# Performance work log

Hardware: AMD Instinct MI355X
Metric: run time of the kernel (lower is better)

The kernel has to match this reference:

```python
import math
import jax, jax.numpy as jnp
import numpy as np

V, BS, L, C, H, B, T = 50257, 2048, 4, 768, 12, 2, 2048
D = C // H


def layer_norm(x, g, b, eps=1e-5):
    m = x.mean(-1, keepdims=True)
    v = ((x - m) ** 2).mean(-1, keepdims=True)
    return (x - m) / jnp.sqrt(v + eps) * g + b


def setup_inputs() -> dict:
    key = jax.random.key(0)
    ks = jax.random.split(key, 10)
    s = 0.02
    inp = {}
    inp["idx"] = jax.random.randint(ks[0], (B, T), 0, V)
    inp["tok_emb"] = jax.random.normal(ks[1], (V, C), jnp.float32) * s
    inp["pos_emb"] = jax.random.normal(ks[2], (BS, C), jnp.float32) * s
    inp["ln1_g"] = jnp.ones((L, C)); inp["ln1_b"] = jnp.zeros((L, C))
    inp["qkv_w"] = jax.random.normal(ks[3], (L, C, 3 * C), jnp.float32) * s
    inp["qkv_b"] = jnp.zeros((L, 3 * C))
    inp["aproj_w"] = jax.random.normal(ks[4], (L, C, C), jnp.float32) * s
    inp["aproj_b"] = jnp.zeros((L, C))
    inp["ln2_g"] = jnp.ones((L, C)); inp["ln2_b"] = jnp.zeros((L, C))
    inp["fc_w"] = jax.random.normal(ks[5], (L, C, 4 * C), jnp.float32) * s
    inp["fc_b"] = jnp.zeros((L, 4 * C))
    inp["mproj_w"] = jax.random.normal(ks[6], (L, 4 * C, C), jnp.float32) * s
    inp["mproj_b"] = jnp.zeros((L, C))
    inp["lnf_g"] = jnp.ones((C,)); inp["lnf_b"] = jnp.zeros((C,))
    inp["head_w"] = jax.random.normal(ks[7], (C, V), jnp.float32) * s
    return inp


def reference(idx, tok_emb, pos_emb, ln1_g, ln1_b, qkv_w, qkv_b, aproj_w, aproj_b,
              ln2_g, ln2_b, fc_w, fc_b, mproj_w, mproj_b, lnf_g, lnf_b, head_w):
    b, t = idx.shape
    x = tok_emb[idx] + pos_emb[:t][None]  # [B,T,C]; dropout p=0 -> identity
    mask = jnp.tril(jnp.ones((t, t), bool))  # causal
    neg_inf = jnp.finfo(x.dtype).min
    n_layer = qkv_w.shape[0]
    for l in range(n_layer):
        h = layer_norm(x, ln1_g[l], ln1_b[l])
        qkv = h @ qkv_w[l] + qkv_b[l]  # [B,T,3C]
        q, k, v = jnp.split(qkv, 3, axis=-1)
        q = q.reshape(b, t, H, D).transpose(0, 2, 1, 3)  # [B,H,T,D]
        k = k.reshape(b, t, H, D).transpose(0, 2, 1, 3)
        v = v.reshape(b, t, H, D).transpose(0, 2, 1, 3)
        att = jnp.einsum('bhqd,bhkd->bhqk', q, k) / math.sqrt(D)
        att = jnp.where(mask, att, neg_inf)
        att = jax.nn.softmax(att, axis=-1)
        y = jnp.einsum('bhqk,bhkd->bhqd', att, v)
        y = y.transpose(0, 2, 1, 3).reshape(b, t, C)
        x = x + (y @ aproj_w[l] + aproj_b[l])
        h2 = layer_norm(x, ln2_g[l], ln2_b[l])
        hid = jax.nn.gelu(h2 @ fc_w[l] + fc_b[l], approximate=False)  # exact erf GELU (torch default)
        x = x + (hid @ mproj_w[l] + mproj_b[l])
    x = layer_norm(x, lnf_g, lnf_b)
    logits = x @ head_w  # [B,T,V]
    return logits
```

## Files before the change

kernel.cpp:

```cpp
#include <hip/hip_runtime.h>
#include <cstdint>
#include <cstddef>

#define Tn 2048
#define Bn 2
#define Hn 12
#define Cn 768
#define Ln 4
#define Vn 50257

typedef unsigned short ushort_t;
typedef __attribute__((ext_vector_type(8))) __bf16 bf16x8;
typedef __attribute__((ext_vector_type(8))) unsigned short u16x8;
typedef __attribute__((ext_vector_type(4))) float f32x4;

static constexpr size_t QKV_ELEMS = (size_t)Bn * Hn * Tn * 64;

__device__ inline unsigned short f2bf(float f) {
  unsigned int u = __float_as_uint(f);
  unsigned int r = (u + 0x7fffu + ((u >> 16) & 1u)) >> 16;
  return (unsigned short)r;
}

__device__ inline f32x4 zero4() { f32x4 z; z[0]=0.f; z[1]=0.f; z[2]=0.f; z[3]=0.f; return z; }

__device__ inline void gload_lds16(const ushort_t* g, ushort_t* l) {
  __builtin_amdgcn_global_load_lds(
      (const __attribute__((address_space(1))) void*)g,
      (__attribute__((address_space(3))) void*)l, 16, 0, 0);
}

__device__ inline int swz_lin() {
  int nbm = gridDim.x;
  int lin = blockIdx.y * nbm + blockIdx.x;
  int nwg = nbm * gridDim.y;
  int q = nwg >> 3, r = nwg & 7, x = lin & 7, p = lin >> 3;
  return (x < r ? x * (q + 1) : r * (q + 1) + (x - r) * q) + p;
}

__global__ __launch_bounds__(256) void embed_kernel(const int* __restrict__ idx,
    const float* __restrict__ tok, const float* __restrict__ pos, float* __restrict__ x) {
  int row = blockIdx.x;
  int t = row & (Tn - 1);
  int token = idx[row];
  const float* tr = tok + (size_t)token * Cn;
  const float* pr = pos + (size_t)t * Cn;
  float* xr = x + (size_t)row * Cn;
  for (int c = threadIdx.x; c < Cn; c += 256) xr[c] = tr[c] + pr[c];
}

__global__ __launch_bounds__(256) void ln_kernel(const float* __restrict__ x,
    const float* __restrict__ gam, const float* __restrict__ bet, ushort_t* __restrict__ out) {
  int row = blockIdx.x;
  const float* xr = x + (size_t)row * Cn;
  float v[3]; float s = 0.f, s2 = 0.f;
  #pragma unroll
  for (int e = 0; e < 3; ++e) { float t = xr[threadIdx.x + e*256]; v[e] = t; s += t; s2 += t*t; }
  #pragma unroll
  for (int off = 32; off >= 1; off >>= 1) { s += __shfl_xor(s, off); s2 += __shfl_xor(s2, off); }
  __shared__ float red[8];
  int w = threadIdx.x >> 6;
  if ((threadIdx.x & 63) == 0) { red[w] = s; red[4 + w] = s2; }
  __syncthreads();
  s  = red[0] + red[1] + red[2] + red[3];
  s2 = red[4] + red[5] + red[6] + red[7];
  float mean = s * (1.f / Cn);
  float var  = s2 * (1.f / Cn) - mean * mean;
  float rstd = rsqrtf(var + 1e-5f);
  ushort_t* orow = out + (size_t)row * Cn;
  #pragma unroll
  for (int e = 0; e < 3; ++e) {
    int c = threadIdx.x + e*256;
    orow[c] = f2bf((v[e] - mean) * rstd * gam[c] + bet[c]);
  }
}

__global__ __launch_bounds__(256) void tcvt_kernel(const float* __restrict__ in,
    ushort_t* __restrict__ out, int K, int N, int Npad) {
  __shared__ float tile[32][33];
  int n0 = blockIdx.x * 32, k0 = blockIdx.y * 32;
  int tx = threadIdx.x, ty = threadIdx.y;
  #pragma unroll
  for (int r = 0; r < 4; ++r) {
    int k = k0 + ty + 8*r;
    int n = n0 + tx;
    tile[ty + 8*r][tx] = (n < N) ? in[(size_t)k * N + n] : 0.f;
  }
  __syncthreads();
  #pragma unroll
  for (int r = 0; r < 4; ++r) {
    int n = n0 + ty + 8*r;
    out[(size_t)n * K + k0 + tx] = f2bf(tile[tx][ty + 8*r]);
  }
}

__global__ __launch_bounds__(256) void vtrans_kernel(const ushort_t* __restrict__ vin,
                                                     ushort_t* __restrict__ vout) {
  __shared__ ushort_t tile[64][65];
  int t0 = blockIdx.x * 64;
  size_t bh = blockIdx.y;
  const ushort_t* src = vin + (bh * Tn + t0) * 64;
  int row = threadIdx.x >> 2, c0 = (threadIdx.x & 3) * 16;
  u16x8 a = *(const u16x8*)&src[(size_t)row * 64 + c0];
  u16x8 b = *(const u16x8*)&src[(size_t)row * 64 + c0 + 8];
  #pragma unroll
  for (int j = 0; j < 8; ++j) { tile[row][c0 + j] = a[j]; tile[row][c0 + 8 + j] = b[j]; }
  __syncthreads();
  int d = threadIdx.x >> 2, tq = (threadIdx.x & 3) * 16;
  u16x8 o0, o1;
  #pragma unroll
  for (int j = 0; j < 8; ++j) { o0[j] = tile[tq + j][d]; o1[j] = tile[tq + 8 + j][d]; }
  ushort_t* dst = vout + (bh * 64 + d) * Tn + t0 + tq;
  *(u16x8*)&dst[0] = o0;
  *(u16x8*)&dst[8] = o1;
}

__global__ __launch_bounds__(512, 2) void gemm256_kernel(
    const ushort_t* __restrict__ A, const ushort_t* __restrict__ Bt,
    const float* __restrict__ bias, float* __restrict__ outp,
    int M, int N, int K) {
  __shared__ ushort_t lds[3 * 16384];
  const int t = threadIdx.x;
  const int w = t >> 6, l = t & 63, lo = l & 15, g = l >> 4;
  const int wm = w >> 2, wn = w & 3;

  int bm, bn;
  {
    int seq = swz_lin();
    int gsz = 8 * gridDim.y;
    int grp = seq / gsz;
    int t2 = seq - grp * gsz;
    bn = t2 >> 3;
    bm = grp * 8 + (t2 & 7);
  }

  const ushort_t* gAb = A  + (size_t)bm * 256 * K;
  const ushort_t* gBb = Bt + (size_t)bn * 256 * K;

  f32x4 acc[8][4];
  #pragma unroll
  for (int i = 0; i < 8; ++i)
    #pragma unroll
    for (int j = 0; j < 4; ++j) acc[i][j] = zero4();

  auto stage = [&](int kt, int buf) {
    const int k0 = kt << 5;
    #pragma unroll
    for (int j = 0; j < 2; ++j) {
      const int q = j * 512 + t;
      const int r = q >> 2;
      const int cc = ((q & 3) ^ ((r >> 1) & 3)) << 3;
      gload_lds16(gAb + (size_t)r * K + k0 + cc,
                  &lds[buf * 16384 + j * 4096 + w * 512]);
      gload_lds16(gBb + (size_t)r * K + k0 + cc,
                  &lds[buf * 16384 + 8192 + j * 4096 + w * 512]);
    }
  };
  const int csw = ((lo >> 1) & 3) << 3;
  auto compute = [&](int buf) {
    const ushort_t* as = &lds[buf * 16384];
    const ushort_t* bs = &lds[buf * 16384 + 8192];
    bf16x8 af[8], bfr[4];
    #pragma unroll
    for (int mi = 0; mi < 8; ++mi)
      af[mi] = *(const bf16x8*)&as[(wm*128 + mi*16 + lo) * 32 + ((g*8) ^ csw)];
    #pragma unroll
    for (int ni = 0; ni < 4; ++ni)
      bfr[ni] = *(const bf16x8*)&bs[(wn*64 + ni*16 + lo) * 32 + ((g*8) ^ csw)];
    __builtin_amdgcn_s_setprio(1);
    #pragma unroll
    for (int mi = 0; mi < 8; ++mi)
      #pragma unroll
      for (int ni = 0; ni < 4; ++ni)
        acc[mi][ni] = __builtin_amdgcn_mfma_f32_16x16x32_bf16(af[mi], bfr[ni], acc[mi][ni], 0, 0, 0);
    __builtin_amdgcn_s_setprio(0);
  };

  const int NK = K >> 5;
  stage(0, 0); stage(1, 1); stage(2, 2);
  asm volatile("s_waitcnt vmcnt(8)" ::: "memory");
  __builtin_amdgcn_s_barrier();

  int buf = 0;
  #pragma unroll 1
  for (int kt = 0; kt < NK; ++kt) {
    compute(buf);
    asm volatile("s_waitcnt lgkmcnt(0)" ::: "memory");
    __builtin_amdgcn_s_barrier();
    if (kt + 3 < NK) {
      stage(kt + 3, buf);
      asm volatile("s_waitcnt vmcnt(8)" ::: "memory");
    } else if (kt + 2 < NK) {
      asm volatile("s_waitcnt vmcnt(4)" ::: "memory");
    } else {
      asm volatile("s_waitcnt vmcnt(0)" ::: "memory");
    }
    __builtin_amdgcn_s_barrier();
    buf = (buf == 2) ? 0 : buf + 1;
  }

  #pragma unroll
  for (int mi = 0; mi < 8; ++mi) {
    #pragma unroll
    for (int ni = 0; ni < 4; ++ni) {
      int colg = bn*256 + wn*64 + ni*16 + lo;
      if (colg < N) {
        float bv = bias ? bias[colg] : 0.f;
        #pragma unroll
        for (int i = 0; i < 4; ++i) {
          int rowg = bm*256 + wm*128 + mi*16 + 4*g + i;
          outp[(size_t)rowg * N + colg] = acc[mi][ni][i] + bv;
        }
      }
    }
  }
}

template<int MODE, int TM>
__global__ __launch_bounds__(256) void gemm_kernel(
    const ushort_t* __restrict__ A, const ushort_t* __restrict__ Bt,
    const float* __restrict__ bias, void* __restrict__ outp,
    const float* __restrict__ res, int M, int N, int K) {
  constexpr int MI = TM / 32;
  constexpr int ABUF = TM * 32;
  __shared__ ushort_t As[2 * ABUF];
  __shared__ ushort_t Bs[2 * 4096];
  const int t = threadIdx.x;
  int bm, bn;
  {
    int seq = swz_lin();
    const int G = 8;
    int NBN = gridDim.y;
    int gsz = G * NBN;
    int grp = seq / gsz;
    int t2 = seq - grp * gsz;
    bn = t2 / G;
    bm = grp * G + (t2 - bn * G);
  }
  const int w = t >> 6, l = t & 63, lo = l & 15, g = l >> 4;
  const int wm = w >> 1, wn = w & 1;

  f32x4 acc[MI][4];
  #pragma unroll
  for (int i = 0; i < MI; ++i)
    #pragma unroll
    for (int j = 0; j < 4; ++j) acc[i][j] = zero4();

  const int srow = t >> 2;
  const int scol = (t & 3) * 8;
  const ushort_t* gA = A  + (size_t)(bm * TM  + srow) * K + scol;
  const ushort_t* gB = Bt + (size_t)(bn * 128 + srow) * K + scol;
  ushort_t* lA = As + w * 512;
  ushort_t* lB = Bs + w * 512;

  auto stage = [&](int buf, int k0) {
    gload_lds16(gA + k0, lA + buf * ABUF);
    if (TM == 128) gload_lds16(gA + (size_t)64 * K + k0, lA + buf * ABUF + 2048);
    gload_lds16(gB + k0, lB + buf * 4096);
    gload_lds16(gB + (size_t)64 * K + k0, lB + buf * 4096 + 2048);
  };
  auto compute = [&](int buf) {
    const ushort_t* as = As + buf * ABUF;
    const ushort_t* bs = Bs + buf * 4096;
    bf16x8 af[MI], bfr[4];
    #pragma unroll
    for (int mi = 0; mi < MI; ++mi)
      af[mi] = *(const bf16x8*)&as[(size_t)(wm*(TM/2) + mi*16 + lo) * 32 + g*8];
    #pragma unroll
    for (int ni = 0; ni < 4; ++ni)
      bfr[ni] = *(const bf16x8*)&bs[(size_t)(wn*64 + ni*16 + lo) * 32 + g*8];
    #pragma unroll
    for (int mi = 0; mi < MI; ++mi)
      #pragma unroll
      for (int ni = 0; ni < 4; ++ni)
        acc[mi][ni] = __builtin_amdgcn_mfma_f32_16x16x32_bf16(af[mi], bfr[ni], acc[mi][ni], 0, 0, 0);
  };

  const int NK = K >> 5;
  stage(0, 0);
  __syncthreads();
  for (int kk = 0; kk < NK - 1; ++kk) {
    stage((kk + 1) & 1, (kk + 1) << 5);
    compute(kk & 1);
    __syncthreads();
  }
  compute((NK - 1) & 1);

  #pragma unroll
  for (int mi = 0; mi < MI; ++mi) {
    #pragma unroll
    for (int ni = 0; ni < 4; ++ni) {
      int colg = bn*128 + wn*64 + ni*16 + lo;
      if (colg < N) {
        float bv = bias ? bias[colg] : 0.f;
        #pragma unroll
        for (int i = 0; i < 4; ++i) {
          int rowg = bm*TM + wm*(TM/2) + mi*16 + 4*g + i;
          float vv = acc[mi][ni][i] + bv;
          if (MODE == 0) {
            ((float*)outp)[(size_t)rowg * N + colg] = vv;
          } else if (MODE == 1) {
            size_t off = (size_t)rowg * N + colg;
            ((float*)outp)[off] = res[off] + vv;
          } else if (MODE == 2) {
            float ge = 0.5f * vv * (1.f + erff(vv * 0.70710678118f));
            ((ushort_t*)outp)[(size_t)rowg * N + colg] = f2bf(ge);
          } else {
            int which = colg / Cn;
            int rem = colg - which * Cn;
            int h = rem >> 6, d = rem & 63;
            int b = rowg >> 11, tt = rowg & (Tn - 1);
            ushort_t* qb = (ushort_t*)outp;
            size_t bh = (size_t)(b * Hn + h);
            size_t off = (bh * Tn + tt) * 64 + d;
            if (which == 0)      qb[off] = f2bf(vv * 0.125f);
            else if (which == 1) qb[QKV_ELEMS + off] = f2bf(vv);
            else                 qb[3*QKV_ELEMS + off] = f2bf(vv);
          }
        }
      }
    }
  }
}

__global__ __launch_bounds__(64) void attn_kernel(const ushort_t* __restrict__ qkvh,
                                                  ushort_t* __restrict__ y) {
  const int l = threadIdx.x;
  const int lo = l & 15, g = l >> 4;
  int nl = swz_lin();
  const int qt = nl & 127;
  const int bh = nl >> 7;
  const int b = bh / Hn, h = bh % Hn;
  const int q0 = qt * 16;
  const ushort_t* Qp = qkvh + (size_t)bh * Tn * 64;
  const ushort_t* Kp = qkvh + QKV_ELEMS + (size_t)bh * Tn * 64;
  const ushort_t* Vt = qkvh + 2*QKV_ELEMS + (size_t)bh * 64 * Tn;

  bf16x8 qf[2];
  #pragma unroll
  for (int ch = 0; ch < 2; ++ch)
    qf[ch] = *(const bf16x8*)&Qp[(size_t)(q0 + lo) * 64 + ch*32 + g*8];

  f32x4 of[4];
  #pragma unroll
  for (int ch = 0; ch < 4; ++ch) of[ch] = zero4();
  float m = -1e30f, lsum = 0.f;
  const int nkv = q0 + 16;
  const bool ghi = (g >= 2);
  const int lg2 = (g & 1) * 32;

  for (int kv0 = 0; kv0 < nkv; kv0 += 32) {
    bf16x8 vf[4];
    #pragma unroll
    for (int ch = 0; ch < 4; ++ch)
      vf[ch] = *(const bf16x8*)&Vt[(size_t)(ch*16 + lo) * Tn + kv0 + g*8];

    float s8[8];
    #pragma unroll
    for (int sub = 0; sub < 2; ++sub) {
      int kvb = kv0 + 16*sub;
      bf16x8 kf[2];
      #pragma unroll
      for (int ch = 0; ch < 2; ++ch)
        kf[ch] = *(const bf16x8*)&Kp[(size_t)(kvb + lo) * 64 + ch*32 + g*8];
      f32x4 st = zero4();
      st = __builtin_amdgcn_mfma_f32_16x16x32_bf16(kf[0], qf[0], st, 0, 0, 0);
      st = __builtin_amdgcn_mfma_f32_16x16x32_bf16(kf[1], qf[1], st, 0, 0, 0);
      #pragma unroll
      for (int i = 0; i < 4; ++i) {
        int kvi = kvb + 4*g + i;
        s8[sub*4 + i] = (kvi <= q0 + lo) ? st[i] : -1e30f;
      }
    }
    float tmax = s8[0];
    #pragma unroll
    for (int j = 1; j < 8; ++j) tmax = fmaxf(tmax, s8[j]);
    tmax = fmaxf(tmax, __shfl_xor(tmax, 16));
    tmax = fmaxf(tmax, __shfl_xor(tmax, 32));
    if (!__all(tmax <= m)) {
      float newm = fmaxf(m, tmax);
      float resc = __expf(m - newm);
      lsum *= resc;
      m = newm;
      #pragma unroll
      for (int i = 0; i < 4; ++i) {
        float rs = __shfl(resc, 4*g + i);
        of[0][i] *= rs; of[1][i] *= rs; of[2][i] *= rs; of[3][i] *= rs;
      }
    }
    float p8[8]; float psum = 0.f;
    #pragma unroll
    for (int j = 0; j < 8; ++j) { p8[j] = __expf(s8[j] - m); psum += p8[j]; }
    psum += __shfl_xor(psum, 16);
    psum += __shfl_xor(psum, 32);
    lsum += psum;
    unsigned int q4[4];
    #pragma unroll
    for (int c = 0; c < 4; ++c)
      asm("v_cvt_pk_bf16_f32 %0, %1, %2" : "=v"(q4[c]) : "v"(p8[2*c]), "v"(p8[2*c+1]));
    union { unsigned int wv[4]; bf16x8 v; } pu;
    #pragma unroll
    for (int j = 0; j < 4; ++j) {
      int srcLane = lo + lg2 + ((j >> 1) << 4);
      unsigned int lo_w = (unsigned int)__shfl((int)q4[j & 1], srcLane);
      unsigned int hi_w = (unsigned int)__shfl((int)q4[2 + (j & 1)], srcLane);
      pu.wv[j] = ghi ? hi_w : lo_w;
    }
    #pragma unroll
    for (int ch = 0; ch < 4; ++ch)
      of[ch] = __builtin_amdgcn_mfma_f32_16x16x32_bf16(pu.v, vf[ch], of[ch], 0, 0, 0);
  }

  #pragma unroll
  for (int i = 0; i < 4; ++i) {
    float li = 1.f / __shfl(lsum, 4*g + i);
    of[0][i] *= li; of[1][i] *= li; of[2][i] *= li; of[3][i] *= li;
  }
  ushort_t* yb = y + ((size_t)b*Tn + q0) * Cn + h*64;
  #pragma unroll
  for (int ch = 0; ch < 4; ++ch)
    #pragma unroll
    for (int i = 0; i < 4; ++i)
      yb[(size_t)(4*g + i) * Cn + ch*16 + lo] = f2bf(of[ch][i]);
}

extern "C" void kernel_launch(void* const* d_in, const int* in_sizes, int n_in,
                              void* d_out, int out_size, void* d_ws, size_t ws_size,
                              hipStream_t stream) {
  const int*   idx     = (const int*)d_in[0];
  const float* tok_emb = (const float*)d_in[1];
  const float* pos_emb = (const float*)d_in[2];
  const float* ln1_g   = (const float*)d_in[3];
  const float* ln1_b   = (const float*)d_in[4];
  const float* qkv_w   = (const float*)d_in[5];
  const float* qkv_b   = (const float*)d_in[6];
  const float* aproj_w = (const float*)d_in[7];
  const float* aproj_b = (const float*)d_in[8];
  const float* ln2_g   = (const float*)d_in[9];
  const float* ln2_b   = (const float*)d_in[10];
  const float* fc_w    = (const float*)d_in[11];
  const float* fc_b    = (const float*)d_in[12];
  const float* mproj_w = (const float*)d_in[13];
  const float* mproj_b = (const float*)d_in[14];
  const float* lnf_g   = (const float*)d_in[15];
  const float* lnf_b   = (const float*)d_in[16];
  const float* head_w  = (const float*)d_in[17];
  float* out = (float*)d_out;

  char* ws = (char*)d_ws;
  float*    x    = (float*)(ws);
  ushort_t* hA   = (ushort_t*)(ws + 12582912);
  ushort_t* hB   = (ushort_t*)(ws + 18874368);
  ushort_t* qkvh = (ushort_t*)(ws + 44040192);
  ushort_t* wT   = (ushort_t*)(ws + 69206016);

  const int M = Bn * Tn;
  dim3 tb(32, 8);

  embed_kernel<<<M, 256, 0, stream>>>(idx, tok_emb, pos_emb, x);
  for (int l = 0; l < Ln; ++l) {
    ln_kernel<<<M, 256, 0, stream>>>(x, ln1_g + l*Cn, ln1_b + l*Cn, hA);
    tcvt_kernel<<<dim3(2304/32, 768/32), tb, 0, stream>>>(qkv_w + (size_t)l*Cn*3*Cn, wT, 768, 2304, 2304);
    gemm_kernel<3,128><<<dim3(M/128, 2304/128), 256, 0, stream>>>(hA, wT, qkv_b + (size_t)l*3*Cn, qkvh, nullptr, M, 2304, 768);
    vtrans_kernel<<<dim3(Tn/64, Bn*Hn), 256, 0, stream>>>(qkvh + 3*QKV_ELEMS, qkvh + 2*QKV_ELEMS);
    attn_kernel<<<dim3(128, Bn*Hn), 64, 0, stream>>>(qkvh, hA);
    tcvt_kernel<<<dim3(768/32, 768/32), tb, 0, stream>>>(aproj_w + (size_t)l*Cn*Cn, wT, 768, 768, 768);
    gemm_kernel<1,64><<<dim3(M/64, 768/128), 256, 0, stream>>>(hA, wT, aproj_b + (size_t)l*Cn, x, x, M, 768, 768);
    ln_kernel<<<M, 256, 0, stream>>>(x, ln2_g + l*Cn, ln2_b + l*Cn, hA);
    tcvt_kernel<<<dim3(3072/32, 768/32), tb, 0, stream>>>(fc_w + (size_t)l*Cn*4*Cn, wT, 768, 3072, 3072);
    gemm_kernel<2,128><<<dim3(M/128, 3072/128), 256, 0, stream>>>(hA, wT, fc_b + (size_t)l*4*Cn, hB, nullptr, M, 3072, 768);
    tcvt_kernel<<<dim3(768/32, 3072/32), tb, 0, stream>>>(mproj_w + (size_t)l*4*Cn*Cn, wT, 3072, 768, 768);
    gemm_kernel<1,64><<<dim3(M/64, 768/128), 256, 0, stream>>>(hB, wT, mproj_b + (size_t)l*Cn, x, x, M, 768, 3072);
  }
  ln_kernel<<<M, 256, 0, stream>>>(x, lnf_g, lnf_b, hA);
  tcvt_kernel<<<dim3(50432/32, 768/32), tb, 0, stream>>>(head_w, wT, 768, Vn, 50432);
  gemm256_kernel<<<dim3(M/256, 50432/256), 512, 0, stream>>>(hA, wT, nullptr, out, M, Vn, 768);
}
```

Before: 1.796 ms.

## Triple-buffer swizzled GEMM pipeline, batch weight conversion, vectorize LN and embed

The layer GEMM moves from a double-buffered LDS loop to a three-stage pipeline. It uses XOR-swizzled LDS layout, explicit vmcnt waits, raw barriers and s_setprio around the MFMA block, aiming to hide load latency and cut LDS bank conflicts. The four per-layer weight transpose/convert launches are merged into one launch writing to fixed offsets. LayerNorm now handles one row per wave with float4 loads and no shared-memory reduction, and the embedding kernel uses float4 loads. The hand-written waitcnt counts depend on how many loads each stage issues, so a wrong count would silently read stale LDS data.

```diff
diff --git a/kernel.cpp b/kernel.cpp
--- a/kernel.cpp
+++ b/kernel.cpp
@@ -12,9 +12,14 @@
 typedef unsigned short ushort_t;
 typedef __attribute__((ext_vector_type(8))) __bf16 bf16x8;
 typedef __attribute__((ext_vector_type(8))) unsigned short u16x8;
+typedef __attribute__((ext_vector_type(4))) unsigned short u16x4;
 typedef __attribute__((ext_vector_type(4))) float f32x4;
 
 static constexpr size_t QKV_ELEMS = (size_t)Bn * Hn * Tn * 64;
+static constexpr size_t OFF_QKV = 0;
+static constexpr size_t OFF_APROJ = 1769472;
+static constexpr size_t OFF_FC = 2359296;
+static constexpr size_t OFF_MPROJ = 4718592;
 
 __device__ inline unsigned short f2bf(float f) {
   unsigned int u = __float_as_uint(f);
@@ -38,40 +43,44 @@
   return (x < r ? x * (q + 1) : r * (q + 1) + (x - r) * q) + p;
 }
 
-__global__ __launch_bounds__(256) void embed_kernel(const int* __restrict__ idx,
+__global__ __launch_bounds__(192) void embed_kernel(const int* __restrict__ idx,
     const float* __restrict__ tok, const float* __restrict__ pos, float* __restrict__ x) {
   int row = blockIdx.x;
   int t = row & (Tn - 1);
   int token = idx[row];
-  const float* tr = tok + (size_t)token * Cn;
-  const float* pr = pos + (size_t)t * Cn;
-  float* xr = x + (size_t)row * Cn;
-  for (int c = threadIdx.x; c < Cn; c += 256) xr[c] = tr[c] + pr[c];
+  const f32x4* tr = (const f32x4*)(tok + (size_t)token * Cn);
+  const f32x4* pr = (const f32x4*)(pos + (size_t)t * Cn);
+  f32x4* xr = (f32x4*)(x + (size_t)row * Cn);
+  xr[threadIdx.x] = tr[threadIdx.x] + pr[threadIdx.x];
 }
 
 __global__ __launch_bounds__(256) void ln_kernel(const float* __restrict__ x,
     const float* __restrict__ gam, const float* __restrict__ bet, ushort_t* __restrict__ out) {
-  int row = blockIdx.x;
-  const float* xr = x + (size_t)row * Cn;
-  float v[3]; float s = 0.f, s2 = 0.f;
-  #pragma unroll
-  for (int e = 0; e < 3; ++e) { float t = xr[threadIdx.x + e*256]; v[e] = t; s += t; s2 += t*t; }
+  const int wv = threadIdx.x >> 6, lane = threadIdx.x & 63;
+  const int row = blockIdx.x * 4 + wv;
+  const f32x4* xr = (const f32x4*)(x + (size_t)row * Cn);
+  f32x4 v[3]; float s = 0.f, s2 = 0.f;
+  #pragma unroll
+  for (int e = 0; e < 3; ++e) {
+    v[e] = xr[lane + e*64];
+    #pragma unroll
+    for (int j = 0; j < 4; ++j) { s += v[e][j]; s2 += v[e][j]*v[e][j]; }
+  }
   #pragma unroll
   for (int off = 32; off >= 1; off >>= 1) { s += __shfl_xor(s, off); s2 += __shfl_xor(s2, off); }
-  __shared__ float red[8];
-  int w = threadIdx.x >> 6;
-  if ((threadIdx.x & 63) == 0) { red[w] = s; red[4 + w] = s2; }
-  __syncthreads();
-  s  = red[0] + red[1] + red[2] + red[3];
-  s2 = red[4] + red[5] + red[6] + red[7];
   float mean = s * (1.f / Cn);
   float var  = s2 * (1.f / Cn) - mean * mean;
   float rstd = rsqrtf(var + 1e-5f);
-  ushort_t* orow = out + (size_t)row * Cn;
+  const f32x4* g4 = (const f32x4*)gam;
+  const f32x4* b4 = (const f32x4*)bet;
+  u16x4* o4 = (u16x4*)(out + (size_t)row * Cn);
   #pragma unroll
   for (int e = 0; e < 3; ++e) {
-    int c = threadIdx.x + e*256;
-    orow[c] = f2bf((v[e] - mean) * rstd * gam[c] + bet[c]);
+    f32x4 gv = g4[lane + e*64], bv = b4[lane + e*64];
+    u16x4 o;
+    #pragma unroll
+    for (int j = 0; j < 4; ++j) o[j] = f2bf((v[e][j] - mean) * rstd * gv[j] + bv[j]);
+    o4[lane + e*64] = o;
   }
 }
 
@@ -92,6 +101,28 @@
     int n = n0 + ty + 8*r;
     out[(size_t)n * K + k0 + tx] = f2bf(tile[tx][ty + 8*r]);
   }
+}
+
+__global__ __launch_bounds__(256) void tcvt4_kernel(const float* __restrict__ qkvp,
+    const float* __restrict__ aprojp, const float* __restrict__ fcp,
+    const float* __restrict__ mprojp, ushort_t* __restrict__ wT) {
+  __shared__ float tile[32][33];
+  int bid = blockIdx.x;
+  const float* in; int K, N, tilesX, local; size_t ooff;
+  if (bid < 1728)      { in = qkvp;   K = 768;  N = 2304; tilesX = 72; ooff = OFF_QKV;   local = bid; }
+  else if (bid < 2304) { in = aprojp; K = 768;  N = 768;  tilesX = 24; ooff = OFF_APROJ; local = bid - 1728; }
+  else if (bid < 4608) { in = fcp;    K = 768;  N = 3072; tilesX = 96; ooff = OFF_FC;    local = bid - 2304; }
+  else                 { in = mprojp; K = 3072; N = 768;  tilesX = 24; ooff = OFF_MPROJ; local = bid - 4608; }
+  int n0 = (local % tilesX) * 32, k0 = (local / tilesX) * 32;
+  int tx = threadIdx.x, ty = threadIdx.y;
+  ushort_t* out = wT + ooff;
+  #pragma unroll
+  for (int r = 0; r < 4; ++r)
+    tile[ty + 8*r][tx] = in[(size_t)(k0 + ty + 8*r) * N + n0 + tx];
+  __syncthreads();
+  #pragma unroll
+  for (int r = 0; r < 4; ++r)
+    out[(size_t)(n0 + ty + 8*r) * K + k0 + tx] = f2bf(tile[tx][ty + 8*r]);
 }
 
 __global__ __launch_bounds__(256) void vtrans_kernel(const ushort_t* __restrict__ vin,
@@ -222,16 +253,16 @@
     const float* __restrict__ bias, void* __restrict__ outp,
     const float* __restrict__ res, int M, int N, int K) {
   constexpr int MI = TM / 32;
-  constexpr int ABUF = TM * 32;
-  __shared__ ushort_t As[2 * ABUF];
-  __shared__ ushort_t Bs[2 * 4096];
+  constexpr int ASZ = TM * 32;
+  constexpr int BUFE = ASZ + 4096;
+  constexpr int LPT = TM/64 + 2;
+  __shared__ ushort_t lds[3 * BUFE];
   const int t = threadIdx.x;
   int bm, bn;
   {
     int seq = swz_lin();
     const int G = 8;
-    int NBN = gridDim.y;
-    int gsz = G * NBN;
+    int gsz = G * gridDim.y;
     int grp = seq / gsz;
     int t2 = seq - grp * gsz;
     bn = t2 / G;
@@ -246,45 +277,71 @@
     #pragma unroll
     for (int j = 0; j < 4; ++j) acc[i][j] = zero4();
 
-  const int srow = t >> 2;
-  const int scol = (t & 3) * 8;
-  const ushort_t* gA = A  + (size_t)(bm * TM  + srow) * K + scol;
-  const ushort_t* gB = Bt + (size_t)(bn * 128 + srow) * K + scol;
-  ushort_t* lA = As + w * 512;
-  ushort_t* lB = Bs + w * 512;
-
-  auto stage = [&](int buf, int k0) {
-    gload_lds16(gA + k0, lA + buf * ABUF);
-    if (TM == 128) gload_lds16(gA + (size_t)64 * K + k0, lA + buf * ABUF + 2048);
-    gload_lds16(gB + k0, lB + buf * 4096);
-    gload_lds16(gB + (size_t)64 * K + k0, lB + buf * 4096 + 2048);
+  const ushort_t* gAb = A  + (size_t)bm * TM * K;
+  const ushort_t* gBb = Bt + (size_t)bn * 128 * K;
+
+  auto stage = [&](int kt, int buf) {
+    const int k0 = kt << 5;
+    #pragma unroll
+    for (int j = 0; j < TM/64; ++j) {
+      const int q = j * 256 + t;
+      const int r = q >> 2;
+      const int cc = ((q & 3) ^ ((r >> 1) & 3)) << 3;
+      gload_lds16(gAb + (size_t)r * K + k0 + cc, &lds[buf*BUFE + (j*256 + w*64)*8]);
+    }
+    #pragma unroll
+    for (int j = 0; j < 2; ++j) {
+      const int q = j * 256 + t;
+      const int r = q >> 2;
+      const int cc = ((q & 3) ^ ((r >> 1) & 3)) << 3;
+      gload_lds16(gBb + (size_t)r * K + k0 + cc, &lds[buf*BUFE + ASZ + (j*256 + w*64)*8]);
+    }
   };
+  const int csw = ((lo >> 1) & 3) << 3;
   auto compute = [&](int buf) {
-    const ushort_t* as = As + buf * ABUF;
-    const ushort_t* bs = Bs + buf * 4096;
+    const ushort_t* as = &lds[buf * BUFE];
+    const ushort_t* bs = &lds[buf * BUFE + ASZ];
     bf16x8 af[MI], bfr[4];
     #pragma unroll
     for (int mi = 0; mi < MI; ++mi)
-      af[mi] = *(const bf16x8*)&as[(size_t)(wm*(TM/2) + mi*16 + lo) * 32 + g*8];
+      af[mi] = *(const bf16x8*)&as[(wm*(TM/2) + mi*16 + lo) * 32 + ((g*8) ^ csw)];
     #pragma unroll
     for (int ni = 0; ni < 4; ++ni)
-      bfr[ni] = *(const bf16x8*)&bs[(size_t)(wn*64 + ni*16 + lo) * 32 + g*8];
+      bfr[ni] = *(const bf16x8*)&bs[(wn*64 + ni*16 + lo) * 32 + ((g*8) ^ csw)];
+    __builtin_amdgcn_s_setprio(1);
     #pragma unroll
     for (int mi = 0; mi < MI; ++mi)
       #pragma unroll
       for (int ni = 0; ni < 4; ++ni)
         acc[mi][ni] = __builtin_amdgcn_mfma_f32_16x16x32_bf16(af[mi], bfr[ni], acc[mi][ni], 0, 0, 0);
+    __builtin_amdgcn_s_setprio(0);
   };
 
   const int NK = K >> 5;
-  stage(0, 0);
-  __syncthreads();
-  for (int kk = 0; kk < NK - 1; ++kk) {
-    stage((kk + 1) & 1, (kk + 1) << 5);
-    compute(kk & 1);
-    __syncthreads();
-  }
-  compute((NK - 1) & 1);
+  stage(0, 0); stage(1, 1); stage(2, 2);
+  if constexpr (LPT == 4) asm volatile("s_waitcnt vmcnt(8)" ::: "memory");
+  else                    asm volatile("s_waitcnt vmcnt(6)" ::: "memory");
+  __builtin_amdgcn_s_barrier();
+
+  int buf = 0;
+  #pragma unroll 1
+  for (int kt = 0; kt < NK; ++kt) {
+    compute(buf);
+    asm volatile("s_waitcnt lgkmcnt(0)" ::: "memory");
+    __builtin_amdgcn_s_barrier();
+    if (kt + 3 < NK) {
+      stage(kt + 3, buf);
+      if constexpr (LPT == 4) asm volatile("s_waitcnt vmcnt(8)" ::: "memory");
+      else                    asm volatile("s_waitcnt vmcnt(6)" ::: "memory");
+    } else if (kt + 2 < NK) {
+      if constexpr (LPT == 4) asm volatile("s_waitcnt vmcnt(4)" ::: "memory");
+      else                    asm volatile("s_waitcnt vmcnt(3)" ::: "memory");
+    } else {
+      asm volatile("s_waitcnt vmcnt(0)" ::: "memory");
+    }
+    __builtin_amdgcn_s_barrier();
+    buf = (buf == 2) ? 0 : buf + 1;
+  }
 
   #pragma unroll
   for (int mi = 0; mi < MI; ++mi) {
@@ -297,9 +354,7 @@
         for (int i = 0; i < 4; ++i) {
           int rowg = bm*TM + wm*(TM/2) + mi*16 + 4*g + i;
           float vv = acc[mi][ni][i] + bv;
-          if (MODE == 0) {
-            ((float*)outp)[(size_t)rowg * N + colg] = vv;
-          } else if (MODE == 1) {
+          if (MODE == 1) {
             size_t off = (size_t)rowg * N + colg;
             ((float*)outp)[off] = res[off] + vv;
           } else if (MODE == 2) {
@@ -457,22 +512,20 @@
   const int M = Bn * Tn;
   dim3 tb(32, 8);
 
-  embed_kernel<<<M, 256, 0, stream>>>(idx, tok_emb, pos_emb, x);
+  embed_kernel<<<M, 192, 0, stream>>>(idx, tok_emb, pos_emb, x);
   for (int l = 0; l < Ln; ++l) {
-    ln_kernel<<<M, 256, 0, stream>>>(x, ln1_g + l*Cn, ln1_b + l*Cn, hA);
-    tcvt_kernel<<<dim3(2304/32, 768/32), tb, 0, stream>>>(qkv_w + (size_t)l*Cn*3*Cn, wT, 768, 2304, 2304);
-    gemm_kernel<3,128><<<dim3(M/128, 2304/128), 256, 0, stream>>>(hA, wT, qkv_b + (size_t)l*3*Cn, qkvh, nullptr, M, 2304, 768);
+    ln_kernel<<<M/4, 256, 0, stream>>>(x, ln1_g + l*Cn, ln1_b + l*Cn, hA);
+    tcvt4_kernel<<<6912, tb, 0, stream>>>(qkv_w + (size_t)l*Cn*3*Cn, aproj_w + (size_t)l*Cn*Cn,
+                                          fc_w + (size_t)l*Cn*4*Cn, mproj_w + (size_t)l*4*Cn*Cn, wT);
+    gemm_kernel<3,128><<<dim3(M/128, 2304/128), 256, 0, stream>>>(hA, wT + OFF_QKV, qkv_b + (size_t)l*3*Cn, qkvh, nullptr, M, 2304, 768);
     vtrans_kernel<<<dim3(Tn/64, Bn*Hn), 256, 0, stream>>>(qkvh + 3*QKV_ELEMS, qkvh + 2*QKV_ELEMS);
     attn_kernel<<<dim3(128, Bn*Hn), 64, 0, stream>>>(qkvh, hA);
-    tcvt_kernel<<<dim3(768/32, 768/32), tb, 0, stream>>>(aproj_w + (size_t)l*Cn*Cn, wT, 768, 768, 768);
-    gemm_kernel<1,64><<<dim3(M/64, 768/128), 256, 0, stream>>>(hA, wT, aproj_b + (size_t)l*Cn, x, x, M, 768, 768);
-    ln_kernel<<<M, 256, 0, stream>>>(x, ln2_g + l*Cn, ln2_b + l*Cn, hA);
-    tcvt_kernel<<<dim3(3072/32, 768/32), tb, 0, stream>>>(fc_w + (size_t)l*Cn*4*Cn, wT, 768, 3072, 3072);
-    gemm_kernel<2,128><<<dim3(M/128, 3072/128), 256, 0, stream>>>(hA, wT, fc_b + (size_t)l*4*Cn, hB, nullptr, M, 3072, 768);
-    tcvt_kernel<<<dim3(768/32, 3072/32), tb, 0, stream>>>(mproj_w + (size_t)l*4*Cn*Cn, wT, 3072, 768, 768);
-    gemm_kernel<1,64><<<dim3(M/64, 768/128), 256, 0, stream>>>(hB, wT, mproj_b + (size_t)l*Cn, x, x, M, 768, 3072);
-  }
-  ln_kernel<<<M, 256, 0, stream>>>(x, lnf_g, lnf_b, hA);
+    gemm_kernel<1,64><<<dim3(M/64, 768/128), 256, 0, stream>>>(hA, wT + OFF_APROJ, aproj_b + (size_t)l*Cn, x, x, M, 768, 768);
+    ln_kernel<<<M/4, 256, 0, stream>>>(x, ln2_g + l*Cn, ln2_b + l*Cn, hA);
+    gemm_kernel<2,128><<<dim3(M/128, 3072/128), 256, 0, stream>>>(hA, wT + OFF_FC, fc_b + (size_t)l*4*Cn, hB, nullptr, M, 3072, 768);
+    gemm_kernel<1,64><<<dim3(M/64, 768/128), 256, 0, stream>>>(hB, wT + OFF_MPROJ, mproj_b + (size_t)l*Cn, x, x, M, 768, 3072);
+  }
+  ln_kernel<<<M/4, 256, 0, stream>>>(x, lnf_g, lnf_b, hA);
   tcvt_kernel<<<dim3(50432/32, 768/32), tb, 0, stream>>>(head_w, wT, 768, Vn, 50432);
   gemm256_kernel<<<dim3(M/256, 50432/256), 512, 0, stream>>>(hA, wT, nullptr, out, M, Vn, 768);
 }
```

Measured after the change: 1.691 ms. -5.9%, faster.
